# Kernel tuning notes

Measured on AMD Instinct MI355X. Metric: run time of the kernel, lower is better.

Reference implementation:

```python
import jax, jax.numpy as jnp
import numpy as np

B, Z, DEG = 4096, 128, 16   # batch (dtPt), totalZONES, avg out-degree
E = Z * DEG                 # number of directed edges = number of tiny MLPs
WV = 0.1                    # WEIGHT_VARIANCE stand-in for normal_(0, WV) init


def setup_inputs() -> dict:
    key = jax.random.key(0)
    ks = jax.random.split(key, 7)
    x = jax.random.normal(ks[0], (B, Z), dtype=jnp.float32)
    # simple graph: each src zone has DEG distinct neighbors (no duplicate edges)
    rng = np.random.default_rng(0)
    dst = np.argsort(rng.random((Z, Z)), axis=1)[:, :DEG].reshape(-1)
    src = np.repeat(np.arange(Z), DEG)
    W1 = jax.random.normal(ks[1], (E, 2, 4), dtype=jnp.float32) * WV
    b1 = jax.random.normal(ks[2], (E, 4), dtype=jnp.float32) * WV
    W2 = jax.random.normal(ks[3], (E, 4, 4), dtype=jnp.float32) * WV
    b2 = jax.random.normal(ks[4], (E, 4), dtype=jnp.float32) * WV
    W3 = jax.random.normal(ks[5], (E, 4), dtype=jnp.float32) * WV  # Linear(4,1) weight, squeezed
    b3 = jax.random.normal(ks[6], (E,), dtype=jnp.float32) * WV
    return {"x": x, "dtPt": B,
            "src": jnp.asarray(src, jnp.int32), "dst": jnp.asarray(dst, jnp.int32),
            "W1": W1, "b1": b1, "W2": W2, "b2": b2, "W3": W3, "b3": b3}


def reference(x, dtPt, src, dst, W1, b1, W2, b2, W3, b3):
    # gather per-edge pair features: [B, E, 2]
    h = jnp.stack([x[:, src], x[:, dst]], axis=-1)
    # per-edge tiny MLP as batched GEMMs (one fused op over all E edges)
    h = jnp.tanh(jnp.einsum('bei,eio->beo', h, W1) + b1)   # [B, E, 4]
    h = jnp.tanh(jnp.einsum('bei,eio->beo', h, W2) + b2)   # [B, E, 4]
    beta = jax.nn.sigmoid(jnp.einsum('bei,ei->be', h, W3) + b3)  # [B, E]
    # scatter into ones-initialized adjacency output [B, Z, Z]
    out = jnp.ones((x.shape[0], Z, Z), dtype=x.dtype)
    return out.at[:, src, dst].set(beta)
```

## Files before the change

kernel.cpp:

```cpp
#include <hip/hip_runtime.h>


#define ZONES 128
#define NB    32

__device__ __forceinline__ float fast_tanh(float v) {
    float e = __expf(2.0f * v);
    return 1.0f - 2.0f * __builtin_amdgcn_rcpf(e + 1.0f);
}
__device__ __forceinline__ float fast_sigmoid(float v) {
    return __builtin_amdgcn_rcpf(1.0f + __expf(-v));
}

__global__ __launch_bounds__(256) void fused_edge_mlp(
    const float* __restrict__ x,
    const int*   __restrict__ dst,
    const float* __restrict__ W1,
    const float* __restrict__ b1,
    const float* __restrict__ W2,
    const float* __restrict__ b2,
    const float* __restrict__ W3,
    const float* __restrict__ b3,
    float* __restrict__ out)
{
    __shared__ float buf[2][2][8 * ZONES];

    const int tid  = threadIdx.x;
    const int rg   = blockIdx.x;
    const int b0   = blockIdx.y * NB;

    const int boff = tid >> 7;
    const int t    = tid & 127;
    const int e    = rg * 128 + t;
    const int srow = rg * 8 + (t >> 4);
    const int dcol = dst[e];

    float w1[8], b1v[4], w2[16], b2v[4], w3[4];
    *(float4*)&w1[0]  = ((const float4*)(W1 + e * 8))[0];
    *(float4*)&w1[4]  = ((const float4*)(W1 + e * 8))[1];
    *(float4*)&b1v[0] = ((const float4*)(b1 + e * 4))[0];
    *(float4*)&w2[0]  = ((const float4*)(W2 + e * 16))[0];
    *(float4*)&w2[4]  = ((const float4*)(W2 + e * 16))[1];
    *(float4*)&w2[8]  = ((const float4*)(W2 + e * 16))[2];
    *(float4*)&w2[12] = ((const float4*)(W2 + e * 16))[3];
    *(float4*)&b2v[0] = ((const float4*)(b2 + e * 4))[0];
    *(float4*)&w3[0]  = ((const float4*)(W3 + e * 4))[0];
    const float b3s = b3[e];

    float4* f4 = (float4*)buf;
    const float4 ones4 = make_float4(1.f, 1.f, 1.f, 1.f);
    #pragma unroll
    for (int i = 0; i < 4; ++i) f4[tid + 256 * i] = ones4;
    __syncthreads();

    float4* out4 = (float4*)out;
    const int scat = boff ? -1 : (t >> 4) * 128 + dcol;

    #pragma unroll 4
    for (int it = 0; it < NB / 2; ++it) {
        const int p = it & 1;
        const int b = b0 + it * 2 + boff;

        const float xs = x[b * ZONES + srow];
        const float xd = x[b * ZONES + dcol];

        float h1[4];
        #pragma unroll
        for (int o = 0; o < 4; ++o)
            h1[o] = fast_tanh(fmaf(xs, w1[o], fmaf(xd, w1[4 + o], b1v[o])));

        float h2[4];
        #pragma unroll
        for (int o = 0; o < 4; ++o) {
            float z = b2v[o];
            #pragma unroll
            for (int k = 0; k < 4; ++k)
                z = fmaf(h1[k], w2[k * 4 + o], z);
            h2[o] = fast_tanh(z);
        }

        float z = b3s;
        #pragma unroll
        for (int o = 0; o < 4; ++o)
            z = fmaf(h2[o], w3[o], z);
        const float beta = fast_sigmoid(z);

        buf[p][boff][(t >> 4) * 128 + dcol] = beta;
        __syncthreads();

        #pragma unroll
        for (int bb = 0; bb < 2; ++bb) {
            const int bw = b0 + it * 2 + bb;
            out4[(size_t)bw * (ZONES * ZONES / 4) + rg * 256 + tid] =
                ((float4*)buf[p][bb])[tid];
        }
    }
    (void)scat;
}

extern "C" void kernel_launch(void* const* d_in, const int* in_sizes, int n_in,
                              void* d_out, int out_size, void* d_ws, size_t ws_size,
                              hipStream_t stream) {
    const float* x   = (const float*)d_in[0];
    const int*   dst = (const int*)  d_in[3];
    const float* W1  = (const float*)d_in[4];
    const float* b1  = (const float*)d_in[5];
    const float* W2  = (const float*)d_in[6];
    const float* b2  = (const float*)d_in[7];
    const float* W3  = (const float*)d_in[8];
    const float* b3  = (const float*)d_in[9];
    float* out = (float*)d_out;

    const int B = in_sizes[0] / ZONES;
    dim3 grid(ZONES / 8, B / NB);
    fused_edge_mlp<<<grid, 256, 0, stream>>>(x, dst, W1, b1, W2, b2, W3, b3, out);
}
```

Baseline: 50.61 us.

## Use packed FMA with rational tanh, stage x in LDS, double batch per block

Replaces the exp-based tanh with a Padé rational approximation evaluated on packed float2 vectors, sharing one reciprocal per pair. The MLP layers now use packed float2 FMAs. Each block's x slice is staged into LDS instead of being gathered from global memory, and the batch per block is doubled. The goal is fewer transcendental and VALU instructions and cheaper x gathers. The cost is larger LDS use, half as many blocks, and some tanh accuracy loss for large inputs.

```diff
diff --git a/kernel.cpp b/kernel.cpp
--- a/kernel.cpp
+++ b/kernel.cpp
@@ -2,12 +2,24 @@
 
 
 #define ZONES 128
-#define NB    32
+#define NB    64
 
-__device__ __forceinline__ float fast_tanh(float v) {
-    float e = __expf(2.0f * v);
-    return 1.0f - 2.0f * __builtin_amdgcn_rcpf(e + 1.0f);
+typedef float f32x2 __attribute__((ext_vector_type(2)));
+typedef float f32x4 __attribute__((ext_vector_type(4)));
+
+__device__ __forceinline__ f32x2 fma2(f32x2 a, f32x2 b, f32x2 c) {
+    return __builtin_elementwise_fma(a, b, c);
 }
+
+__device__ __forceinline__ f32x2 tanh2(f32x2 v) {
+    const f32x2 s = v * v;
+    const f32x2 n = v * fma2(s, fma2(s, (f32x2)21.0f, (f32x2)1260.0f), (f32x2)10395.0f);
+    const f32x2 d = fma2(s, fma2(s, s + (f32x2)210.0f, (f32x2)4725.0f), (f32x2)10395.0f);
+    const float r = __builtin_amdgcn_rcpf(d.x * d.y);
+    f32x2 dsw; dsw.x = d.y; dsw.y = d.x;
+    return (n * dsw) * (f32x2)r;
+}
+
 __device__ __forceinline__ float fast_sigmoid(float v) {
     return __builtin_amdgcn_rcpf(1.0f + __expf(-v));
 }
@@ -23,6 +35,7 @@
     const float* __restrict__ b3,
     float* __restrict__ out)
 {
+    __shared__ float x_lds[NB * ZONES];
     __shared__ float buf[2][2][8 * ZONES];
 
     const int tid  = threadIdx.x;
@@ -35,67 +48,74 @@
     const int srow = rg * 8 + (t >> 4);
     const int dcol = dst[e];
 
-    float w1[8], b1v[4], w2[16], b2v[4], w3[4];
-    *(float4*)&w1[0]  = ((const float4*)(W1 + e * 8))[0];
-    *(float4*)&w1[4]  = ((const float4*)(W1 + e * 8))[1];
-    *(float4*)&b1v[0] = ((const float4*)(b1 + e * 4))[0];
-    *(float4*)&w2[0]  = ((const float4*)(W2 + e * 16))[0];
-    *(float4*)&w2[4]  = ((const float4*)(W2 + e * 16))[1];
-    *(float4*)&w2[8]  = ((const float4*)(W2 + e * 16))[2];
-    *(float4*)&w2[12] = ((const float4*)(W2 + e * 16))[3];
-    *(float4*)&b2v[0] = ((const float4*)(b2 + e * 4))[0];
-    *(float4*)&w3[0]  = ((const float4*)(W3 + e * 4))[0];
-    const float b3s = b3[e];
+    const f32x4 w1q0 = ((const f32x4*)(W1 + e * 8))[0];
+    const f32x4 w1q1 = ((const f32x4*)(W1 + e * 8))[1];
+    const f32x4 b1q  = ((const f32x4*)(b1 + e * 4))[0];
+    const f32x4 w2k0 = ((const f32x4*)(W2 + e * 16))[0];
+    const f32x4 w2k1 = ((const f32x4*)(W2 + e * 16))[1];
+    const f32x4 w2k2 = ((const f32x4*)(W2 + e * 16))[2];
+    const f32x4 w2k3 = ((const f32x4*)(W2 + e * 16))[3];
+    const f32x4 b2q  = ((const f32x4*)(b2 + e * 4))[0];
+    const f32x4 w3q  = ((const f32x4*)(W3 + e * 4))[0];
+    const float b3s  = b3[e];
 
-    float4* f4 = (float4*)buf;
-    const float4 ones4 = make_float4(1.f, 1.f, 1.f, 1.f);
+    const f32x4* xg = (const f32x4*)(x + (size_t)b0 * ZONES);
+    f32x4* xl = (f32x4*)x_lds;
+    #pragma unroll
+    for (int i = 0; i < 8; ++i) xl[tid + 256 * i] = xg[tid + 256 * i];
+
+    f32x4* f4 = (f32x4*)buf;
+    const f32x4 ones4 = {1.f, 1.f, 1.f, 1.f};
     #pragma unroll
     for (int i = 0; i < 4; ++i) f4[tid + 256 * i] = ones4;
     __syncthreads();
 
-    float4* out4 = (float4*)out;
-    const int scat = boff ? -1 : (t >> 4) * 128 + dcol;
+    f32x4* out4 = (f32x4*)out;
 
-    #pragma unroll 4
+    #pragma unroll 2
     for (int it = 0; it < NB / 2; ++it) {
-        const int p = it & 1;
-        const int b = b0 + it * 2 + boff;
+        const int p  = it & 1;
+        const int br = 2 * it + boff;
 
-        const float xs = x[b * ZONES + srow];
-        const float xd = x[b * ZONES + dcol];
+        const float xs = x_lds[br * ZONES + srow];
+        const float xd = x_lds[br * ZONES + dcol];
 
-        float h1[4];
-        #pragma unroll
-        for (int o = 0; o < 4; ++o)
-            h1[o] = fast_tanh(fmaf(xs, w1[o], fmaf(xd, w1[4 + o], b1v[o])));
+        f32x2 xs2; xs2.x = xs; xs2.y = xs;
+        f32x2 xd2; xd2.x = xd; xd2.y = xd;
 
-        float h2[4];
-        #pragma unroll
-        for (int o = 0; o < 4; ++o) {
-            float z = b2v[o];
-            #pragma unroll
-            for (int k = 0; k < 4; ++k)
-                z = fmaf(h1[k], w2[k * 4 + o], z);
-            h2[o] = fast_tanh(z);
-        }
+        f32x2 z01 = fma2(xs2, w1q0.xy, fma2(xd2, w1q1.xy, b1q.xy));
+        f32x2 z23 = fma2(xs2, w1q0.zw, fma2(xd2, w1q1.zw, b1q.zw));
+        const f32x2 h01 = tanh2(z01);
+        const f32x2 h23 = tanh2(z23);
 
-        float z = b3s;
-        #pragma unroll
-        for (int o = 0; o < 4; ++o)
-            z = fmaf(h2[o], w3[o], z);
-        const float beta = fast_sigmoid(z);
+        f32x2 hb;
+        f32x2 y01 = b2q.xy, y23 = b2q.zw;
+        hb.x = h01.x; hb.y = h01.x;
+        y01 = fma2(hb, w2k0.xy, y01); y23 = fma2(hb, w2k0.zw, y23);
+        hb.x = h01.y; hb.y = h01.y;
+        y01 = fma2(hb, w2k1.xy, y01); y23 = fma2(hb, w2k1.zw, y23);
+        hb.x = h23.x; hb.y = h23.x;
+        y01 = fma2(hb, w2k2.xy, y01); y23 = fma2(hb, w2k2.zw, y23);
+        hb.x = h23.y; hb.y = h23.y;
+        y01 = fma2(hb, w2k3.xy, y01); y23 = fma2(hb, w2k3.zw, y23);
 
-        buf[p][boff][(t >> 4) * 128 + dcol] = beta;
+        const f32x2 g01 = tanh2(y01);
+        const f32x2 g23 = tanh2(y23);
+
+        f32x2 acc0; acc0.x = b3s; acc0.y = 0.f;
+        const f32x2 acc = fma2(g01, w3q.xy, fma2(g23, w3q.zw, acc0));
+        const float beta = fast_sigmoid(acc.x + acc.y);
+
+        buf[p][boff][(t >> 4) * ZONES + dcol] = beta;
         __syncthreads();
 
         #pragma unroll
         for (int bb = 0; bb < 2; ++bb) {
-            const int bw = b0 + it * 2 + bb;
+            const int bw = b0 + 2 * it + bb;
             out4[(size_t)bw * (ZONES * ZONES / 4) + rg * 256 + tid] =
-                ((float4*)buf[p][bb])[tid];
+                ((f32x4*)buf[p][bb])[tid];
         }
     }
-    (void)scat;
 }
 
 extern "C" void kernel_launch(void* const* d_in, const int* in_sizes, int n_in,
```

Measured after the change: 53.17 us. +5.1%, slower.
